# Kernel tuning notes

Hardware: AMD Instinct MI355X
Metric: run time of the kernel (lower is better)

Reference implementation:

```python
import jax, jax.numpy as jnp
import numpy as np

H_DIM_EXP = 25  # n = 2**25 = 33,554,432

def setup_inputs() -> dict:
    key = jax.random.key(0)
    x = jax.random.normal(key, (2 ** H_DIM_EXP,), dtype=jnp.float32)
    return {"x": x, "h_dim_exp": H_DIM_EXP}

def reference(x, h_dim_exp):
    # Fast Walsh-Hadamard transform. The original views x as [1,2,2,...,2,1]
    # and applies a (+,-) butterfly along each of the log2(n) axes-of-size-2.
    # Butterfly stages on distinct bits commute, so we process bits from low
    # to high with rank-3 reshapes instead of a rank-(exp+2) tensor.
    y = x
    for i in range(h_dim_exp):
        y = y.reshape(-1, 2, 2 ** i)        # (n/2^{i+1}, 2, 2^i)
        a, b = y[:, 0, :], y[:, 1, :]
        y = jnp.stack([a + b, a - b], axis=1)
    return y.reshape(x.shape)
```

## Files before the change

### kernel.cpp

```cpp
#include <hip/hip_runtime.h>


__device__ __forceinline__ void bfly(float4& a, float4& b) {
  float ax = a.x, ay = a.y, az = a.z, aw = a.w;
  a.x = ax + b.x; a.y = ay + b.y; a.z = az + b.z; a.w = aw + b.w;
  b.x = ax - b.x; b.y = ay - b.y; b.z = az - b.z; b.w = aw - b.w;
}

__device__ __forceinline__ void cross4(float4 (&v)[16]) {
#pragma unroll
  for (int m = 0; m < 4; ++m) {
#pragma unroll
    for (int k = 0; k < 16; ++k) {
      if (!(k & (1 << m))) bfly(v[k], v[k | (1 << m)]);
    }
  }
}

__global__ __launch_bounds__(256) void wht_pass1(const float4* __restrict__ in4,
                                                 float4* __restrict__ out4) {
  __shared__ float4 lds[4096];
  const int t = threadIdx.x;
  const int base4 = (int)blockIdx.x << 12;
  float4 v[16];
#pragma unroll
  for (int k = 0; k < 16; ++k) v[k] = in4[base4 + t + (k << 8)];
#pragma unroll
  for (int k = 0; k < 16; ++k) {
    float4 a = v[k];
    float s0 = a.x + a.y, d0 = a.x - a.y, s1 = a.z + a.w, d1 = a.z - a.w;
    v[k].x = s0 + s1; v[k].y = d0 + d1; v[k].z = s0 - s1; v[k].w = d0 - d1;
  }
  cross4(v);

#pragma unroll
  for (int k = 0; k < 16; ++k) { int q = t + (k << 8); lds[q ^ ((q >> 4) & 15)] = v[k]; }
  __syncthreads();
#pragma unroll
  for (int u = 0; u < 16; ++u) { int q = u + (t << 4); v[u] = lds[q ^ ((q >> 4) & 15)]; }
  cross4(v);

#pragma unroll
  for (int u = 0; u < 16; ++u) { int q = u + (t << 4); lds[q ^ ((q >> 4) & 15)] = v[u]; }
  __syncthreads();
  const int c0 = t & 15, c1 = t >> 4;
#pragma unroll
  for (int u = 0; u < 16; ++u) {
    int q = c0 + (u << 4) + (c1 << 8);
    v[u] = lds[q ^ ((q >> 4) & 15)];
  }
  cross4(v);

#pragma unroll
  for (int u = 0; u < 16; ++u) out4[base4 + c0 + (u << 4) + (c1 << 8)] = v[u];
}

__global__ __launch_bounds__(1024, 4) void wht_pass2(float4* __restrict__ b4) {
  __shared__ float4 lds[4096];
  const int t = threadIdx.x;
  const int cb4 = (int)blockIdx.x << 3;
  const int c4 = t & 7;
  const int cc = t & 1;
  const int qt = (t >> 1) & 3;
  const int rlo = t >> 3;
  float4 v[16];
#pragma unroll
  for (int k = 0; k < 16; ++k)
    v[k] = b4[((long)(rlo + (k << 7)) << 12) + cb4 + c4];
  cross4(v);

#pragma unroll 1
  for (int r4 = 0; r4 < 4; ++r4) {
    __syncthreads();
    if (qt == r4) {
#pragma unroll
      for (int k = 0; k < 16; ++k) {
        int q = ((rlo + (k << 7)) << 1) | cc;
        lds[q ^ (((q >> 8) & 3) << 1)] = v[k];
      }
    }
    __syncthreads();
    if (qt == r4) {
#pragma unroll
      for (int rb = 0; rb < 16; ++rb) {
        int q = ((rb + (rlo << 4)) << 1) | cc;
        v[rb] = lds[q ^ (((q >> 8) & 3) << 1)];
      }
    }
  }
  cross4(v);

  const int rlowC = (t >> 3) & 15;
  const int rhi4C = (t & 1) | (((t >> 7) & 7) << 1);
#pragma unroll 1
  for (int r4 = 0; r4 < 4; ++r4) {
    __syncthreads();
    if (qt == r4) {
#pragma unroll
      for (int rb = 0; rb < 16; ++rb) {
        int q = ((rb + (rlo << 4)) << 1) | cc;
        lds[q ^ (((q >> 8) & 3) << 1)] = v[rb];
      }
    }
    __syncthreads();
    if (qt == r4) {
#pragma unroll
      for (int i = 0; i < 16; ++i) {
        int rm = i & 7, c = i >> 3;
        int r = rlowC + (rm << 4) + (rhi4C << 7);
        int q = (r << 1) | c;
        v[i] = lds[q ^ (((q >> 8) & 3) << 1)];
      }
    }
  }
#pragma unroll
  for (int m = 0; m < 3; ++m) {
#pragma unroll
    for (int i = 0; i < 16; ++i) {
      if (!(i & (1 << m))) bfly(v[i], v[i | (1 << m)]);
    }
  }

#pragma unroll
  for (int i = 0; i < 16; ++i) {
    int rm = i & 7, c = i >> 3;
    int r = rlowC + (rm << 4) + (rhi4C << 7);
    b4[((long)r << 12) + cb4 + (qt << 1) + c] = v[i];
  }
}

extern "C" void kernel_launch(void* const* d_in, const int* in_sizes, int n_in,
                              void* d_out, int out_size, void* d_ws, size_t ws_size,
                              hipStream_t stream) {
  (void)in_sizes; (void)n_in; (void)d_ws; (void)ws_size; (void)out_size;
  const float* x = (const float*)d_in[0];
  float* out = (float*)d_out;
  wht_pass1<<<2048, 256, 0, stream>>>((const float4*)x, (float4*)out);
  wht_pass2<<<512, 1024, 0, stream>>>((float4*)out);
}
```

Baseline: 307.2 us.

## Restructure WHT pass2 to 512 threads with 32 values each and nontemporal memory ops

Pass2 now uses 512-thread blocks, each thread holding 32 float4 values. Five butterfly stages run in registers before any LDS exchange, and the old serialized four-round quarter-thread LDS shuffles are replaced by two half-buffer exchanges through a 128KB LDS tile. Global loads and stores in both passes use nontemporal builtins to avoid cache pollution on this streaming workload. The larger register and LDS footprint per thread lowers occupancy, and the LDS indexing drops the old XOR swizzle, which may introduce bank conflicts.

```diff
diff --git a/kernel.cpp b/kernel.cpp
--- a/kernel.cpp
+++ b/kernel.cpp
@@ -1,5 +1,16 @@
 #include <hip/hip_runtime.h>
 
+
+typedef float vf4 __attribute__((ext_vector_type(4)));
+
+__device__ __forceinline__ float4 ntload(const float4* p) {
+  vf4 r = __builtin_nontemporal_load(reinterpret_cast<const vf4*>(p));
+  return *reinterpret_cast<float4*>(&r);
+}
+__device__ __forceinline__ void ntstore(float4* p, float4 v) {
+  __builtin_nontemporal_store(*reinterpret_cast<vf4*>(&v),
+                              reinterpret_cast<vf4*>(p));
+}
 
 __device__ __forceinline__ void bfly(float4& a, float4& b) {
   float ax = a.x, ay = a.y, az = a.z, aw = a.w;
@@ -24,7 +35,8 @@
   const int base4 = (int)blockIdx.x << 12;
   float4 v[16];
 #pragma unroll
-  for (int k = 0; k < 16; ++k) v[k] = in4[base4 + t + (k << 8)];
+  for (int k = 0; k < 16; ++k)
+    v[k] = ntload(&in4[base4 + t + (k << 8)]);
 #pragma unroll
   for (int k = 0; k < 16; ++k) {
     float4 a = v[k];
@@ -55,77 +67,68 @@
   for (int u = 0; u < 16; ++u) out4[base4 + c0 + (u << 4) + (c1 << 8)] = v[u];
 }
 
-__global__ __launch_bounds__(1024, 4) void wht_pass2(float4* __restrict__ b4) {
-  __shared__ float4 lds[4096];
+__global__ __launch_bounds__(512) void wht_pass2(float4* __restrict__ b4) {
+  __shared__ float4 lds[8192];
   const int t = threadIdx.x;
   const int cb4 = (int)blockIdx.x << 3;
   const int c4 = t & 7;
-  const int cc = t & 1;
-  const int qt = (t >> 1) & 3;
   const int rlo = t >> 3;
-  float4 v[16];
+  float4 v[32];
 #pragma unroll
-  for (int k = 0; k < 16; ++k)
-    v[k] = b4[((long)(rlo + (k << 7)) << 12) + cb4 + c4];
-  cross4(v);
+  for (int k = 0; k < 32; ++k)
+    v[k] = ntload(&b4[((rlo + (k << 6)) << 12) + cb4 + c4]);
 
-#pragma unroll 1
-  for (int r4 = 0; r4 < 4; ++r4) {
+#pragma unroll
+  for (int m = 0; m < 5; ++m) {
+#pragma unroll
+    for (int k = 0; k < 32; ++k)
+      if (!(k & (1 << m))) bfly(v[k], v[k | (1 << m)]);
+  }
+
+  const int rhi6 = t >> 3;
+
+#pragma unroll
+  for (int b = 0; b < 2; ++b) {
+    if (b) __syncthreads();
+#pragma unroll
+    for (int k16 = 0; k16 < 16; ++k16)
+      lds[((rlo + (k16 << 6)) << 3) + c4] = v[(b << 4) | k16];
     __syncthreads();
-    if (qt == r4) {
 #pragma unroll
-      for (int k = 0; k < 16; ++k) {
-        int q = ((rlo + (k << 7)) << 1) | cc;
-        lds[q ^ (((q >> 8) & 3) << 1)] = v[k];
-      }
-    }
+    for (int j16 = 0; j16 < 16; ++j16)
+      v[(b << 4) | j16] = lds[((j16 + (rhi6 << 4)) << 3) + c4];
+  }
+  cross4(*reinterpret_cast<float4(*)[16]>(&v[0]));
+  cross4(*reinterpret_cast<float4(*)[16]>(&v[16]));
+
+#pragma unroll
+  for (int b = 0; b < 2; ++b) {
+    if (b) __syncthreads();
+#pragma unroll
+    for (int j16 = 0; j16 < 16; ++j16)
+      lds[((j16 + (rhi6 << 4)) << 3) + c4] = v[(b << 4) | j16];
     __syncthreads();
-    if (qt == r4) {
 #pragma unroll
-      for (int rb = 0; rb < 16; ++rb) {
-        int q = ((rb + (rlo << 4)) << 1) | cc;
-        v[rb] = lds[q ^ (((q >> 8) & 3) << 1)];
-      }
-    }
-  }
-  cross4(v);
-
-  const int rlowC = (t >> 3) & 15;
-  const int rhi4C = (t & 1) | (((t >> 7) & 7) << 1);
-#pragma unroll 1
-  for (int r4 = 0; r4 < 4; ++r4) {
-    __syncthreads();
-    if (qt == r4) {
-#pragma unroll
-      for (int rb = 0; rb < 16; ++rb) {
-        int q = ((rb + (rlo << 4)) << 1) | cc;
-        lds[q ^ (((q >> 8) & 3) << 1)] = v[rb];
-      }
-    }
-    __syncthreads();
-    if (qt == r4) {
-#pragma unroll
-      for (int i = 0; i < 16; ++i) {
-        int rm = i & 7, c = i >> 3;
-        int r = rlowC + (rm << 4) + (rhi4C << 7);
-        int q = (r << 1) | c;
-        v[i] = lds[q ^ (((q >> 8) & 3) << 1)];
-      }
+    for (int i = 0; i < 16; ++i) {
+      int rowkey = ((i >> 2) & 3) | (((t >> 3) & 3) << 2) | ((i & 3) << 4) |
+                   ((t >> 5) << 6);
+      v[(b << 4) | i] = lds[(rowkey << 3) + c4];
     }
   }
 #pragma unroll
-  for (int m = 0; m < 3; ++m) {
+  for (int m = 0; m < 2; ++m) {
 #pragma unroll
-    for (int i = 0; i < 16; ++i) {
+    for (int i = 0; i < 32; ++i)
       if (!(i & (1 << m))) bfly(v[i], v[i | (1 << m)]);
-    }
   }
 
 #pragma unroll
-  for (int i = 0; i < 16; ++i) {
-    int rm = i & 7, c = i >> 3;
-    int r = rlowC + (rm << 4) + (rhi4C << 7);
-    b4[((long)r << 12) + cb4 + (qt << 1) + c] = v[i];
+  for (int i2 = 0; i2 < 32; ++i2) {
+    int b = i2 >> 4, i = i2 & 15;
+    int rowkey = ((i >> 2) & 3) | (((t >> 3) & 3) << 2) | ((i & 3) << 4) |
+                 ((t >> 5) << 6);
+    int row = rowkey | (b << 10);
+    ntstore(&b4[(row << 12) + cb4 + c4], v[i2]);
   }
 }
 
@@ -136,5 +139,5 @@
   const float* x = (const float*)d_in[0];
   float* out = (float*)d_out;
   wht_pass1<<<2048, 256, 0, stream>>>((const float4*)x, (float4*)out);
-  wht_pass2<<<512, 1024, 0, stream>>>((float4*)out);
+  wht_pass2<<<512, 512, 0, stream>>>((float4*)out);
 }
```

Result: faster. 295.0 us (-4.0%).

## Restructure pass1 to 512 threads with radix-8 stages and nontemporal loads

Applied to the files above, without the earlier changes.

Pass1 now uses 512 threads per block, each holding 8 float4 instead of 16. The 12 cross-float4 bits are split into four radix-8 stages instead of three radix-16 stages, which adds one more LDS round trip and barrier. The aim is to halve per-thread register pressure and raise occupancy and memory-level parallelism in this bandwidth-bound pass. Input loads also become nontemporal to reduce cache pollution. The cost is extra shared-memory traffic and synchronisation.

```diff
diff --git a/kernel.cpp b/kernel.cpp
--- a/kernel.cpp
+++ b/kernel.cpp
@@ -1,5 +1,12 @@
 #include <hip/hip_runtime.h>
 
+
+typedef float vf4 __attribute__((ext_vector_type(4)));
+
+__device__ __forceinline__ float4 ntload(const float4* p) {
+  vf4 r = __builtin_nontemporal_load(reinterpret_cast<const vf4*>(p));
+  return *reinterpret_cast<float4*>(&r);
+}
 
 __device__ __forceinline__ void bfly(float4& a, float4& b) {
   float ax = a.x, ay = a.y, az = a.z, aw = a.w;
@@ -17,42 +24,72 @@
   }
 }
 
-__global__ __launch_bounds__(256) void wht_pass1(const float4* __restrict__ in4,
+__device__ __forceinline__ void cross3(float4 (&v)[8]) {
+#pragma unroll
+  for (int m = 0; m < 3; ++m) {
+#pragma unroll
+    for (int k = 0; k < 8; ++k) {
+      if (!(k & (1 << m))) bfly(v[k], v[k | (1 << m)]);
+    }
+  }
+}
+
+__global__ __launch_bounds__(512) void wht_pass1(const float4* __restrict__ in4,
                                                  float4* __restrict__ out4) {
   __shared__ float4 lds[4096];
   const int t = threadIdx.x;
   const int base4 = (int)blockIdx.x << 12;
-  float4 v[16];
+  float4 v[8];
 #pragma unroll
-  for (int k = 0; k < 16; ++k) v[k] = in4[base4 + t + (k << 8)];
+  for (int k = 0; k < 8; ++k)
+    v[k] = ntload(&in4[base4 + t + (k << 9)]);
 #pragma unroll
-  for (int k = 0; k < 16; ++k) {
+  for (int k = 0; k < 8; ++k) {
     float4 a = v[k];
     float s0 = a.x + a.y, d0 = a.x - a.y, s1 = a.z + a.w, d1 = a.z - a.w;
     v[k].x = s0 + s1; v[k].y = d0 + d1; v[k].z = s0 - s1; v[k].w = d0 - d1;
   }
-  cross4(v);
+  cross3(v);
 
 #pragma unroll
-  for (int k = 0; k < 16; ++k) { int q = t + (k << 8); lds[q ^ ((q >> 4) & 15)] = v[k]; }
+  for (int k = 0; k < 8; ++k) { int s = t + (k << 9); lds[s ^ ((s >> 3) & 7)] = v[k]; }
   __syncthreads();
 #pragma unroll
-  for (int u = 0; u < 16; ++u) { int q = u + (t << 4); v[u] = lds[q ^ ((q >> 4) & 15)]; }
-  cross4(v);
+  for (int u = 0; u < 8; ++u) { int s = u + (t << 3); v[u] = lds[s ^ ((s >> 3) & 7)]; }
+  cross3(v);
 
 #pragma unroll
-  for (int u = 0; u < 16; ++u) { int q = u + (t << 4); lds[q ^ ((q >> 4) & 15)] = v[u]; }
+  for (int u = 0; u < 8; ++u) { int s = u + (t << 3); lds[s ^ ((s >> 3) & 7)] = v[u]; }
   __syncthreads();
-  const int c0 = t & 15, c1 = t >> 4;
+  {
+    const int c0 = t & 7, c1 = t >> 3;
 #pragma unroll
-  for (int u = 0; u < 16; ++u) {
-    int q = c0 + (u << 4) + (c1 << 8);
-    v[u] = lds[q ^ ((q >> 4) & 15)];
+    for (int u = 0; u < 8; ++u) {
+      int s = c0 + (u << 3) + (c1 << 6);
+      v[u] = lds[s ^ ((s >> 3) & 7)];
+    }
   }
-  cross4(v);
+  cross3(v);
+
+  {
+    const int c0 = t & 7, c1 = t >> 3;
+#pragma unroll
+    for (int u = 0; u < 8; ++u) {
+      int s = c0 + (u << 3) + (c1 << 6);
+      lds[s ^ ((s >> 3) & 7)] = v[u];
+    }
+  }
+  __syncthreads();
+  const int c0b = t & 63, c1b = t >> 6;
+#pragma unroll
+  for (int u = 0; u < 8; ++u) {
+    int s = c0b + (u << 6) + (c1b << 9);
+    v[u] = lds[s ^ ((s >> 3) & 7)];
+  }
+  cross3(v);
 
 #pragma unroll
-  for (int u = 0; u < 16; ++u) out4[base4 + c0 + (u << 4) + (c1 << 8)] = v[u];
+  for (int u = 0; u < 8; ++u) out4[base4 + c0b + (u << 6) + (c1b << 9)] = v[u];
 }
 
 __global__ __launch_bounds__(1024, 4) void wht_pass2(float4* __restrict__ b4) {
@@ -135,6 +172,6 @@
   (void)in_sizes; (void)n_in; (void)d_ws; (void)ws_size; (void)out_size;
   const float* x = (const float*)d_in[0];
   float* out = (float*)d_out;
-  wht_pass1<<<2048, 256, 0, stream>>>((const float4*)x, (float4*)out);
+  wht_pass1<<<2048, 512, 0, stream>>>((const float4*)x, (float4*)out);
   wht_pass2<<<512, 1024, 0, stream>>>((float4*)out);
 }
```

Result: faster. 296.6 us (-3.5%).
